# Kernel optimization log

Measured on AMD Instinct MI355X. Metric: run time of the kernel, lower is better.

The kernel has to match this reference:

```python
import jax, jax.numpy as jnp
import numpy as np

N_NODES = 100000
N_EDGES = 50000
NNZ = 1600000
D_IN = 128
D_OUT = 128  # heads(8) * out_channels(16)


def setup_inputs() -> dict:
    key = jax.random.key(0)
    k1, k2, k3, k4 = jax.random.split(key, 4)
    X = jax.random.normal(k1, (N_NODES, D_IN), dtype=jnp.float32)
    W = jax.random.normal(k2, (D_IN, D_OUT), dtype=jnp.float32) * (1.0 / np.sqrt(D_IN))
    eps = jnp.zeros((1,), dtype=jnp.float32)
    vertex = jax.random.randint(k3, (NNZ,), 0, N_NODES, dtype=jnp.int32)
    edges = jax.random.randint(k4, (NNZ,), 0, N_EDGES, dtype=jnp.int32)
    return {"X": X, "W": W, "eps": eps, "vertex": vertex, "edges": edges,
            "num_edges": N_EDGES}


def reference(X, W, eps, vertex, edges, num_edges):
    N = X.shape[0]
    Xp = X @ W                                   # [N, D_OUT] linear proj (no bias)
    Xve = Xp[vertex]                             # [nnz, D_OUT] vertex -> incidence gather
    Xe = jax.ops.segment_sum(Xve, edges, num_segments=num_edges)   # [E, D_OUT] first_aggregate='sum'
    Xev = Xe[edges]                              # [nnz, D_OUT] edge -> incidence gather
    Xv = jax.ops.segment_sum(Xev, vertex, num_segments=N)          # [N, D_OUT]
    out = (1.0 + eps) * Xp + Xv                  # GIN combine with learnable eps (eps is [1], broadcasts)
    return jax.nn.gelu(out, approximate=False)   # torch F.gelu default = exact erf
```

## Files before the change

kernel.cpp:

```cpp
#include <hip/hip_runtime.h>
#include <math.h>

#define NN 100000
#define NE 50000
#define NSEG (NE + NN)
#define DD 128

#define NBE 196
#define NBV 391
#define NB  (NBE + NBV)
#define CAP_E 8960
#define CAP_V 4608

typedef short bf16x8 __attribute__((ext_vector_type(8)));
typedef float f32x4 __attribute__((ext_vector_type(4)));
typedef float v2f __attribute__((ext_vector_type(2)));

static __device__ __forceinline__ float gelu_exact(float x) {
  return 0.5f * x * (1.0f + erff(x * 0.70710678118654752f));
}

static __device__ __forceinline__ int bucket_base(int g) {
  return (g < NBE) ? g * CAP_E : NBE * CAP_E + (g - NBE) * CAP_V;
}

static __device__ __forceinline__ void acc2(v2f& a, unsigned u) {
  union { unsigned i; float f; } lo, hi;
  lo.i = u << 16;
  hi.i = u & 0xFFFF0000u;
  v2f t;
  t.x = lo.f;
  t.y = hi.f;
  a += t;
}

static __device__ __forceinline__ unsigned pack_bf16x2(float a, float b) {
  unsigned ua = __float_as_uint(a), ub = __float_as_uint(b);
  ua = (ua + 0x7FFFu + ((ua >> 16) & 1u)) >> 16;
  ub = (ub + 0x7FFFu + ((ub >> 16) & 1u)) >> 16;
  return ua | (ub << 16);
}

static __device__ __forceinline__ unsigned short bf16_rne(float a) {
  unsigned ua = __float_as_uint(a);
  ua = (ua + 0x7FFFu + ((ua >> 16) & 1u)) >> 16;
  return (unsigned short)ua;
}

__global__ void k_zero(int* __restrict__ gcur) {
  int g = blockIdx.x * blockDim.x + threadIdx.x;
  if (g < NB) gcur[g] = bucket_base(g);
}

__global__ void k_wt(const float* __restrict__ W, unsigned short* __restrict__ Wt) {
  int idx = blockIdx.x * 256 + threadIdx.x;
  int k = idx >> 7, n = idx & 127;
  Wt[n * 128 + k] = bf16_rne(W[idx]);
}

__global__ __launch_bounds__(256) void k_gemm(const float* __restrict__ X,
                                              const unsigned short* __restrict__ Wt,
                                              float* __restrict__ Xp,
                                              unsigned short* __restrict__ Xb2) {
  const int tid = threadIdx.x;
  const int w = tid >> 6;
  const int l = tid & 63;
  const int lm = l & 15;
  const int lk = l >> 4;
  const int R = blockIdx.x * 64 + w * 16;
  const int arow = R + lm;
  const bool rowok = arow < NN;
  const float4* __restrict__ X4 = (const float4*)X;
  const uint4* __restrict__ Wt4 = (const uint4*)Wt;

  f32x4 acc[8];
#pragma unroll
  for (int t = 0; t < 8; ++t) acc[t] = (f32x4)(0.f);

  for (int c = 0; c < 4; ++c) {
    const int k0 = c * 32 + lk * 8;
    float4 x0 = make_float4(0.f, 0.f, 0.f, 0.f), x1 = x0;
    if (rowok) {
      x0 = X4[arow * 32 + (k0 >> 2)];
      x1 = X4[arow * 32 + (k0 >> 2) + 1];
    }
    union { bf16x8 v; uint4 u; } a;
    a.u.x = pack_bf16x2(x0.x, x0.y);
    a.u.y = pack_bf16x2(x0.z, x0.w);
    a.u.z = pack_bf16x2(x1.x, x1.y);
    a.u.w = pack_bf16x2(x1.z, x1.w);
#pragma unroll
    for (int t = 0; t < 8; ++t) {
      union { bf16x8 v; uint4 u; } b;
      b.u = Wt4[(t * 16 + lm) * 16 + c * 4 + lk];
      acc[t] = __builtin_amdgcn_mfma_f32_16x16x32_bf16(a.v, b.v, acc[t], 0, 0, 0);
    }
  }

  const int drow = R + lk * 4;
#pragma unroll
  for (int r = 0; r < 4; ++r) {
    const int row = drow + r;
    if (row < NN) {
#pragma unroll
      for (int t = 0; t < 8; ++t) {
        const float v = acc[t][r];
        const int col = t * 16 + lm;
        Xp[row * 128 + col] = v;
        Xb2[row * 128 + col] = bf16_rne(v);
      }
    }
  }
}

__global__ __launch_bounds__(256) void k_pass1(const int* __restrict__ vertex,
                                               const int* __restrict__ edges,
                                               int* __restrict__ gcur,
                                               int* __restrict__ S, int nnz) {
  __shared__ int hist[NB];
  const int tid = threadIdx.x;
  for (int b = tid; b < NB; b += 256) hist[b] = 0;
  __syncthreads();
  const int base = blockIdx.x * 4096;
#pragma unroll
  for (int k = 0; k < 16; ++k) {
    int i = base + tid + k * 256;
    if (i < nnz) {
      atomicAdd(&hist[edges[i] >> 8], 1);
      atomicAdd(&hist[NBE + (vertex[i] >> 8)], 1);
    }
  }
  __syncthreads();
  for (int b = tid; b < NB; b += 256) {
    int c = hist[b];
    hist[b] = c ? atomicAdd(&gcur[b], c) : 0;
  }
  __syncthreads();
#pragma unroll
  for (int k = 0; k < 16; ++k) {
    int i = base + tid + k * 256;
    if (i < nnz) {
      int e = edges[i], v = vertex[i];
      int pe = atomicAdd(&hist[e >> 8], 1);
      S[pe] = ((e & 255) << 17) | v;
      int pv = atomicAdd(&hist[NBE + (v >> 8)], 1);
      S[pv] = ((v & 255) << 17) | e;
    }
  }
}

__global__ __launch_bounds__(1024) void k_bscan(const int* __restrict__ gcur,
                                                int* __restrict__ gbase) {
  __shared__ int s[1024];
  const int g = threadIdx.x;
  int cnt = 0;
  if (g < NB) cnt = gcur[g] - bucket_base(g);
  s[g] = cnt;
  __syncthreads();
  for (int off = 1; off < 1024; off <<= 1) {
    int y = (g >= off) ? s[g - off] : 0;
    __syncthreads();
    s[g] += y;
    __syncthreads();
  }
  if (g < NB) gbase[g] = s[g] - cnt;
}

__global__ __launch_bounds__(256) void k_pass2(const int* __restrict__ gcur,
                                               const int* __restrict__ gbase,
                                               const int* __restrict__ S,
                                               int* __restrict__ L,
                                               int* __restrict__ O) {
  __shared__ int offs[257];
  __shared__ int cur[256];
  __shared__ int scratch[CAP_E];
  const int g = blockIdx.x;
  const int tid = threadIdx.x;
  const bool isE = g < NBE;
  const int sstart = bucket_base(g);
  int nit = gcur[g] - sstart;
  const int cap = isE ? CAP_E : CAP_V;
  if (nit > cap) nit = cap;
  const int s0 = isE ? (g << 8) : ((g - NBE) << 8);
  const int segN = min(256, (isE ? NE : NN) - s0);
  const int obase = isE ? s0 : NE + s0;
  const int dbase = gbase[g];
  for (int k = tid; k < 257; k += 256) offs[k] = 0;
  __syncthreads();
  for (int t = tid; t < nit; t += 256) atomicAdd(&offs[(S[sstart + t] >> 17) + 1], 1);
  __syncthreads();
  for (int off = 1; off < 256; off <<= 1) {
    int y = (tid >= off) ? offs[tid + 1 - off] : 0;
    __syncthreads();
    offs[tid + 1] += y;
    __syncthreads();
  }
  cur[tid] = offs[tid];
  __syncthreads();
  for (int t = tid; t < nit; t += 256) {
    int u = S[sstart + t];
    int r = atomicAdd(&cur[u >> 17], 1);
    scratch[r] = u & 0x1FFFF;
  }
  __syncthreads();
  for (int t = tid; t < nit; t += 256) L[dbase + t] = scratch[t];
  for (int k = tid; k <= segN; k += 256) O[obase + k] = dbase + offs[k];
}

__global__ __launch_bounds__(256) void k_edge_agg(const unsigned* __restrict__ Xb2,
                                                  const int* __restrict__ O,
                                                  const int* __restrict__ L,
                                                  unsigned* __restrict__ Xe2) {
  const int e = blockIdx.x * 4 + (threadIdx.x >> 6);
  const int lane = threadIdx.x & 63;
  const int q = lane >> 4;
  const int ql = lane & 15;
  const int start = O[e];
  const int end = O[e + 1];
  const uint4* __restrict__ P = (const uint4*)Xb2;
  v2f a[4];
#pragma unroll
  for (int k = 0; k < 4; ++k) a[k] = (v2f)(0.f);
  int j = start + q;
  for (; j + 4 < end; j += 8) {
    uint4 u0 = P[L[j] * 16 + ql];
    uint4 u1 = P[L[j + 4] * 16 + ql];
    acc2(a[0], u0.x); acc2(a[1], u0.y); acc2(a[2], u0.z); acc2(a[3], u0.w);
    acc2(a[0], u1.x); acc2(a[1], u1.y); acc2(a[2], u1.z); acc2(a[3], u1.w);
  }
  if (j < end) {
    uint4 u0 = P[L[j] * 16 + ql];
    acc2(a[0], u0.x); acc2(a[1], u0.y); acc2(a[2], u0.z); acc2(a[3], u0.w);
  }
#pragma unroll
  for (int k = 0; k < 4; ++k) {
    float u0 = a[k].x, u1 = a[k].y;
    u0 += __shfl_xor(u0, 16); u0 += __shfl_xor(u0, 32);
    u1 += __shfl_xor(u1, 16); u1 += __shfl_xor(u1, 32);
    a[k].x = u0; a[k].y = u1;
  }
  float s0 = (q == 0) ? a[0].x : (q == 1) ? a[1].x : (q == 2) ? a[2].x : a[3].x;
  float s1 = (q == 0) ? a[0].y : (q == 1) ? a[1].y : (q == 2) ? a[2].y : a[3].y;
  Xe2[e * 64 + ql * 4 + q] = pack_bf16x2(s0, s1);
}

__global__ __launch_bounds__(256) void k_vert_agg(const unsigned* __restrict__ Xe2,
                                                  const int* __restrict__ O,
                                                  const int* __restrict__ L,
                                                  const float* __restrict__ eps,
                                                  float* __restrict__ XpOut) {
  const int v = blockIdx.x * 4 + (threadIdx.x >> 6);
  const int lane = threadIdx.x & 63;
  const int q = lane >> 4;
  const int ql = lane & 15;
  const int start = O[NE + v];
  const int end = O[NE + v + 1];
  const uint4* __restrict__ Q = (const uint4*)Xe2;
  v2f a[4];
#pragma unroll
  for (int k = 0; k < 4; ++k) a[k] = (v2f)(0.f);
  int j = start + q;
  for (; j + 4 < end; j += 8) {
    uint4 u0 = Q[L[j] * 16 + ql];
    uint4 u1 = Q[L[j + 4] * 16 + ql];
    acc2(a[0], u0.x); acc2(a[1], u0.y); acc2(a[2], u0.z); acc2(a[3], u0.w);
    acc2(a[0], u1.x); acc2(a[1], u1.y); acc2(a[2], u1.z); acc2(a[3], u1.w);
  }
  if (j < end) {
    uint4 u0 = Q[L[j] * 16 + ql];
    acc2(a[0], u0.x); acc2(a[1], u0.y); acc2(a[2], u0.z); acc2(a[3], u0.w);
  }
#pragma unroll
  for (int k = 0; k < 4; ++k) {
    float u0 = a[k].x, u1 = a[k].y;
    u0 += __shfl_xor(u0, 16); u0 += __shfl_xor(u0, 32);
    u1 += __shfl_xor(u1, 16); u1 += __shfl_xor(u1, 32);
    a[k].x = u0; a[k].y = u1;
  }
  float s0 = (q == 0) ? a[0].x : (q == 1) ? a[1].x : (q == 2) ? a[2].x : a[3].x;
  float s1 = (q == 0) ? a[0].y : (q == 1) ? a[1].y : (q == 2) ? a[2].y : a[3].y;
  float2* __restrict__ P2 = (float2*)XpOut;
  const int fi = v * 64 + ql * 4 + q;
  float2 x = P2[fi];
  const float sc = 1.0f + eps[0];
  x.x = gelu_exact(fmaf(sc, x.x, s0));
  x.y = gelu_exact(fmaf(sc, x.y, s1));
  P2[fi] = x;
}

extern "C" void kernel_launch(void* const* d_in, const int* in_sizes, int n_in,
                              void* d_out, int out_size, void* d_ws, size_t ws_size,
                              hipStream_t stream) {
  const float* X = (const float*)d_in[0];
  const float* W = (const float*)d_in[1];
  const float* eps = (const float*)d_in[2];
  const int* vertex = (const int*)d_in[3];
  const int* edges = (const int*)d_in[4];
  const int nnz = in_sizes[3];

  char* ws = (char*)d_ws;
  size_t off = 0;
  auto alloc = [&](size_t bytes) -> void* {
    void* p = ws + off;
    off = (off + bytes + 255) & ~(size_t)255;
    return p;
  };
  const size_t stagingB = ((size_t)NBE * CAP_E + (size_t)NBV * CAP_V) * 4;
  const size_t xbB = (size_t)NN * DD * 2;
  void* A = alloc(xbB > stagingB ? xbB : stagingB);
  int* S = (int*)A;
  unsigned short* Xb2 = (unsigned short*)A;
  unsigned* Xe2 = (unsigned*)alloc((size_t)NE * DD * 2);
  int* L = (int*)alloc((size_t)2 * nnz * sizeof(int));
  int* O = (int*)alloc((size_t)(NSEG + 1) * sizeof(int));
  int* gcur = (int*)alloc((size_t)NB * sizeof(int));
  int* gbase = (int*)alloc((size_t)NB * sizeof(int));
  unsigned short* Wt = (unsigned short*)alloc((size_t)DD * DD * 2);
  if (off > ws_size) return;

  float* Xp = (float*)d_out;

  k_zero<<<3, 256, 0, stream>>>(gcur);
  k_wt<<<64, 256, 0, stream>>>(W, Wt);
  k_pass1<<<(nnz + 4095) / 4096, 256, 0, stream>>>(vertex, edges, gcur, S, nnz);
  k_bscan<<<1, 1024, 0, stream>>>(gcur, gbase);
  k_pass2<<<NB, 256, 0, stream>>>(gcur, gbase, S, L, O);
  k_gemm<<<(NN + 63) / 64, 256, 0, stream>>>(X, Wt, Xp, Xb2);
  k_edge_agg<<<NE / 4, 256, 0, stream>>>((const unsigned*)Xb2, O, L, Xe2);
  k_vert_agg<<<NN / 4, 256, 0, stream>>>(Xe2, O, L, eps, Xp);
}
```

Measured before the change: 324.9 us.

## Drop fp32 Xp write, merge init kernels, inline bucket scan, unroll gathers

Several changes land together. The GEMM no longer writes the fp32 projection; the vertex aggregation rebuilds the self term from the bf16 copy and writes the output with nontemporal stores. The zero and transpose kernels become one launch, and the bucket scan kernel is removed: each pass2 block now sums the preceding bucket counts itself. The gather loops in both aggregation kernels are unrolled to four outstanding loads. This saves a 51 MB fp32 write and read plus two launches, but the self term now uses bf16 precision and pass2 repeats a prefix reduction of up to 587 entries in every block.

Result: faster. 308.6 us (-5.0%).

```diff
diff --git a/kernel.cpp b/kernel.cpp
--- a/kernel.cpp
+++ b/kernel.cpp
@@ -47,20 +47,22 @@
   return (unsigned short)ua;
 }
 
-__global__ void k_zero(int* __restrict__ gcur) {
-  int g = blockIdx.x * blockDim.x + threadIdx.x;
-  if (g < NB) gcur[g] = bucket_base(g);
-}
-
-__global__ void k_wt(const float* __restrict__ W, unsigned short* __restrict__ Wt) {
-  int idx = blockIdx.x * 256 + threadIdx.x;
-  int k = idx >> 7, n = idx & 127;
-  Wt[n * 128 + k] = bf16_rne(W[idx]);
+__global__ __launch_bounds__(256) void k_init(int* __restrict__ gcur,
+                                              const float* __restrict__ W,
+                                              unsigned short* __restrict__ Wt) {
+  const int b = blockIdx.x;
+  if (b < 64) {
+    int idx = b * 256 + threadIdx.x;
+    int k = idx >> 7, n = idx & 127;
+    Wt[n * 128 + k] = bf16_rne(W[idx]);
+  } else {
+    int g = (b - 64) * 256 + threadIdx.x;
+    if (g < NB) gcur[g] = bucket_base(g);
+  }
 }
 
 __global__ __launch_bounds__(256) void k_gemm(const float* __restrict__ X,
                                               const unsigned short* __restrict__ Wt,
-                                              float* __restrict__ Xp,
                                               unsigned short* __restrict__ Xb2) {
   const int tid = threadIdx.x;
   const int w = tid >> 6;
@@ -70,7 +72,7 @@
   const int R = blockIdx.x * 64 + w * 16;
   const int arow = R + lm;
   const bool rowok = arow < NN;
-  const float4* __restrict__ X4 = (const float4*)X;
+  const f32x4* __restrict__ X4 = (const f32x4*)X;
   const uint4* __restrict__ Wt4 = (const uint4*)Wt;
 
   f32x4 acc[8];
@@ -79,10 +81,10 @@
 
   for (int c = 0; c < 4; ++c) {
     const int k0 = c * 32 + lk * 8;
-    float4 x0 = make_float4(0.f, 0.f, 0.f, 0.f), x1 = x0;
+    f32x4 x0 = (f32x4)(0.f), x1 = (f32x4)(0.f);
     if (rowok) {
-      x0 = X4[arow * 32 + (k0 >> 2)];
-      x1 = X4[arow * 32 + (k0 >> 2) + 1];
+      x0 = __builtin_nontemporal_load(&X4[arow * 32 + (k0 >> 2)]);
+      x1 = __builtin_nontemporal_load(&X4[arow * 32 + (k0 >> 2) + 1]);
     }
     union { bf16x8 v; uint4 u; } a;
     a.u.x = pack_bf16x2(x0.x, x0.y);
@@ -104,10 +106,7 @@
     if (row < NN) {
 #pragma unroll
       for (int t = 0; t < 8; ++t) {
-        const float v = acc[t][r];
-        const int col = t * 16 + lm;
-        Xp[row * 128 + col] = v;
-        Xb2[row * 128 + col] = bf16_rne(v);
+        Xb2[row * 128 + t * 16 + lm] = bf16_rne(acc[t][r]);
       }
     }
   }
@@ -149,25 +148,7 @@
   }
 }
 
-__global__ __launch_bounds__(1024) void k_bscan(const int* __restrict__ gcur,
-                                                int* __restrict__ gbase) {
-  __shared__ int s[1024];
-  const int g = threadIdx.x;
-  int cnt = 0;
-  if (g < NB) cnt = gcur[g] - bucket_base(g);
-  s[g] = cnt;
-  __syncthreads();
-  for (int off = 1; off < 1024; off <<= 1) {
-    int y = (g >= off) ? s[g - off] : 0;
-    __syncthreads();
-    s[g] += y;
-    __syncthreads();
-  }
-  if (g < NB) gbase[g] = s[g] - cnt;
-}
-
 __global__ __launch_bounds__(256) void k_pass2(const int* __restrict__ gcur,
-                                               const int* __restrict__ gbase,
                                                const int* __restrict__ S,
                                                int* __restrict__ L,
                                                int* __restrict__ O) {
@@ -176,6 +157,18 @@
   __shared__ int scratch[CAP_E];
   const int g = blockIdx.x;
   const int tid = threadIdx.x;
+  int part = 0;
+  for (int i = tid; i < g; i += 256) part += gcur[i] - bucket_base(i);
+  cur[tid] = part;
+  __syncthreads();
+#pragma unroll
+  for (int s2 = 128; s2 > 0; s2 >>= 1) {
+    if (tid < s2) cur[tid] += cur[tid + s2];
+    __syncthreads();
+  }
+  const int dbase = cur[0];
+  __syncthreads();
+
   const bool isE = g < NBE;
   const int sstart = bucket_base(g);
   int nit = gcur[g] - sstart;
@@ -184,7 +177,6 @@
   const int s0 = isE ? (g << 8) : ((g - NBE) << 8);
   const int segN = min(256, (isE ? NE : NN) - s0);
   const int obase = isE ? s0 : NE + s0;
-  const int dbase = gbase[g];
   for (int k = tid; k < 257; k += 256) offs[k] = 0;
   __syncthreads();
   for (int t = tid; t < nit; t += 256) atomicAdd(&offs[(S[sstart + t] >> 17) + 1], 1);
@@ -222,11 +214,22 @@
 #pragma unroll
   for (int k = 0; k < 4; ++k) a[k] = (v2f)(0.f);
   int j = start + q;
-  for (; j + 4 < end; j += 8) {
+  for (; j + 12 < end; j += 16) {
     uint4 u0 = P[L[j] * 16 + ql];
     uint4 u1 = P[L[j + 4] * 16 + ql];
+    uint4 u2 = P[L[j + 8] * 16 + ql];
+    uint4 u3 = P[L[j + 12] * 16 + ql];
     acc2(a[0], u0.x); acc2(a[1], u0.y); acc2(a[2], u0.z); acc2(a[3], u0.w);
     acc2(a[0], u1.x); acc2(a[1], u1.y); acc2(a[2], u1.z); acc2(a[3], u1.w);
+    acc2(a[0], u2.x); acc2(a[1], u2.y); acc2(a[2], u2.z); acc2(a[3], u2.w);
+    acc2(a[0], u3.x); acc2(a[1], u3.y); acc2(a[2], u3.z); acc2(a[3], u3.w);
+  }
+  if (j + 4 < end) {
+    uint4 u0 = P[L[j] * 16 + ql];
+    uint4 u1 = P[L[j + 4] * 16 + ql];
+    acc2(a[0], u0.x); acc2(a[1], u0.y); acc2(a[2], u0.z); acc2(a[3], u0.w);
+    acc2(a[0], u1.x); acc2(a[1], u1.y); acc2(a[2], u1.z); acc2(a[3], u1.w);
+    j += 8;
   }
   if (j < end) {
     uint4 u0 = P[L[j] * 16 + ql];
@@ -248,7 +251,8 @@
                                                   const int* __restrict__ O,
                                                   const int* __restrict__ L,
                                                   const float* __restrict__ eps,
-                                                  float* __restrict__ XpOut) {
+                                                  const unsigned* __restrict__ Xb2,
+                                                  float* __restrict__ out) {
   const int v = blockIdx.x * 4 + (threadIdx.x >> 6);
   const int lane = threadIdx.x & 63;
   const int q = lane >> 4;
@@ -260,11 +264,22 @@
 #pragma unroll
   for (int k = 0; k < 4; ++k) a[k] = (v2f)(0.f);
   int j = start + q;
-  for (; j + 4 < end; j += 8) {
+  for (; j + 12 < end; j += 16) {
     uint4 u0 = Q[L[j] * 16 + ql];
     uint4 u1 = Q[L[j + 4] * 16 + ql];
+    uint4 u2 = Q[L[j + 8] * 16 + ql];
+    uint4 u3 = Q[L[j + 12] * 16 + ql];
     acc2(a[0], u0.x); acc2(a[1], u0.y); acc2(a[2], u0.z); acc2(a[3], u0.w);
     acc2(a[0], u1.x); acc2(a[1], u1.y); acc2(a[2], u1.z); acc2(a[3], u1.w);
+    acc2(a[0], u2.x); acc2(a[1], u2.y); acc2(a[2], u2.z); acc2(a[3], u2.w);
+    acc2(a[0], u3.x); acc2(a[1], u3.y); acc2(a[2], u3.z); acc2(a[3], u3.w);
+  }
+  if (j + 4 < end) {
+    uint4 u0 = Q[L[j] * 16 + ql];
+    uint4 u1 = Q[L[j + 4] * 16 + ql];
+    acc2(a[0], u0.x); acc2(a[1], u0.y); acc2(a[2], u0.z); acc2(a[3], u0.w);
+    acc2(a[0], u1.x); acc2(a[1], u1.y); acc2(a[2], u1.z); acc2(a[3], u1.w);
+    j += 8;
   }
   if (j < end) {
     uint4 u0 = Q[L[j] * 16 + ql];
@@ -279,13 +294,16 @@
   }
   float s0 = (q == 0) ? a[0].x : (q == 1) ? a[1].x : (q == 2) ? a[2].x : a[3].x;
   float s1 = (q == 0) ? a[0].y : (q == 1) ? a[1].y : (q == 2) ? a[2].y : a[3].y;
-  float2* __restrict__ P2 = (float2*)XpOut;
-  const int fi = v * 64 + ql * 4 + q;
-  float2 x = P2[fi];
+  unsigned su = Xb2[v * 64 + ql * 4 + q];
+  union { unsigned i; float f; } plo, phi;
+  plo.i = su << 16;
+  phi.i = su & 0xFFFF0000u;
   const float sc = 1.0f + eps[0];
-  x.x = gelu_exact(fmaf(sc, x.x, s0));
-  x.y = gelu_exact(fmaf(sc, x.y, s1));
-  P2[fi] = x;
+  v2f x;
+  x.x = gelu_exact(fmaf(sc, plo.f, s0));
+  x.y = gelu_exact(fmaf(sc, phi.f, s1));
+  v2f* __restrict__ P2 = (v2f*)out;
+  __builtin_nontemporal_store(x, &P2[v * 64 + ql * 4 + q]);
 }
 
 extern "C" void kernel_launch(void* const* d_in, const int* in_sizes, int n_in,
@@ -314,18 +332,14 @@
   int* L = (int*)alloc((size_t)2 * nnz * sizeof(int));
   int* O = (int*)alloc((size_t)(NSEG + 1) * sizeof(int));
   int* gcur = (int*)alloc((size_t)NB * sizeof(int));
-  int* gbase = (int*)alloc((size_t)NB * sizeof(int));
   unsigned short* Wt = (unsigned short*)alloc((size_t)DD * DD * 2);
   if (off > ws_size) return;
 
-  float* Xp = (float*)d_out;
-
-  k_zero<<<3, 256, 0, stream>>>(gcur);
-  k_wt<<<64, 256, 0, stream>>>(W, Wt);
+  k_init<<<67, 256, 0, stream>>>(gcur, W, Wt);
   k_pass1<<<(nnz + 4095) / 4096, 256, 0, stream>>>(vertex, edges, gcur, S, nnz);
-  k_bscan<<<1, 1024, 0, stream>>>(gcur, gbase);
-  k_pass2<<<NB, 256, 0, stream>>>(gcur, gbase, S, L, O);
-  k_gemm<<<(NN + 63) / 64, 256, 0, stream>>>(X, Wt, Xp, Xb2);
+  k_pass2<<<NB, 256, 0, stream>>>(gcur, S, L, O);
+  k_gemm<<<(NN + 63) / 64, 256, 0, stream>>>(X, Wt, Xb2);
   k_edge_agg<<<NE / 4, 256, 0, stream>>>((const unsigned*)Xb2, O, L, Xe2);
-  k_vert_agg<<<NN / 4, 256, 0, stream>>>(Xe2, O, L, eps, Xp);
-}
+  k_vert_agg<<<NN / 4, 256, 0, stream>>>(Xe2, O, L, eps, (const unsigned*)Xb2,
+                                         (float*)d_out);
+}
```
